# Kernel optimization log

Hardware: AMD Instinct MI355X
Metric: run time of the kernel (lower is better)

The kernel has to match this reference:

```python
import jax, jax.numpy as jnp
import numpy as np

TOKENS_PER_LAYER = 16  # v in rearrange 'b l (a v) -> b l a v'


def setup_inputs() -> dict:
    key = jax.random.key(0)
    k1, k2 = jax.random.split(key)
    vocab, embed_dim = 1024, 256
    x = jax.random.normal(k1, (64, 32, embed_dim * TOKENS_PER_LAYER), dtype=jnp.float32)
    # nn.Embedding init: uniform(-1/vocab, 1/vocab)
    emb_weight = jax.random.uniform(k2, (vocab, embed_dim), dtype=jnp.float32,
                                    minval=-1.0 / vocab, maxval=1.0 / vocab)
    return {"x": x, "emb_weight": emb_weight}


def reference(x, emb_weight):
    v = TOKENS_PER_LAYER
    b, l, av = x.shape
    a = av // v  # embed_dim
    # rearrange 'b l (a v) -> b l a v'
    z = x.reshape(b, l, a, v)
    # rearrange 'b l a v -> (b l v) a'
    z_flat = z.transpose(0, 1, 3, 2).reshape(b * l * v, a)
    # pairwise squared L2 distance via sum-of-squares + GEMM: [N, vocab]
    dist = (jnp.sum(z_flat * z_flat, axis=1, keepdims=True)
            + jnp.sum(emb_weight * emb_weight, axis=1)
            - 2.0 * (z_flat @ emb_weight.T))
    tokens = jnp.argmin(dist, axis=-1)  # [N] int
    # embedding gather, then rearrange '(b l v) e -> b l e v'
    z_q = emb_weight[tokens].reshape(b, l, v, a).transpose(0, 1, 3, 2)
    # straight-through decoder input: z + sg(z_q - z)
    decoder_input = z + jax.lax.stop_gradient(z_q - z)
    tokens = tokens.reshape(b, l, v)
    return z_q, decoder_input, tokens
```

## Files before the change

### kernel.cpp

```cpp
#include <hip/hip_runtime.h>


#define A_DIM 256
#define VOCAB 1024
#define NROWS 32768
#define ZQ_ELEMS ((size_t)8388608)
#define TAU_C 3.0e-4f
#define TAU_F 2.0e-4f

typedef _Float16 f16x8 __attribute__((ext_vector_type(8)));
typedef _Float16 f16x4 __attribute__((ext_vector_type(4)));
typedef float f32x4 __attribute__((ext_vector_type(4)));

#define WS_EHT   ((size_t)0)
#define WS_ZH    ((size_t)524288)
#define WS_ESQ   ((size_t)17301504)
#define WS_ZSQ   ((size_t)17305600)
#define WS_RINFO ((size_t)17436672)
#define WS_NEED  ((size_t)17960960)


__global__ __launch_bounds__(256) void prep_fused(const float* __restrict__ x,
                                                  const float* __restrict__ emb,
                                                  _Float16* __restrict__ zh,
                                                  float* __restrict__ zsq,
                                                  float* __restrict__ esq,
                                                  _Float16* __restrict__ eht) {
    __shared__ float raw[A_DIM * 17];
    const int tid = threadIdx.x;
    if (blockIdx.x >= 2048) {
        const int blk = blockIdx.x - 2048;
        const int j = blk * 16 + (tid & 15);
        const int sub = tid >> 4;
        const float4* row = (const float4*)(emb + (size_t)j * A_DIM);
        #pragma unroll
        for (int t = 0; t < 2; ++t) {
            int kb = sub * 2 + t;
            float4 e0 = row[kb * 2], e1 = row[kb * 2 + 1];
            f16x8 hh;
            hh[0] = (_Float16)e0.x; hh[1] = (_Float16)e0.y; hh[2] = (_Float16)e0.z; hh[3] = (_Float16)e0.w;
            hh[4] = (_Float16)e1.x; hh[5] = (_Float16)e1.y; hh[6] = (_Float16)e1.z; hh[7] = (_Float16)e1.w;
            *(f16x8*)(eht + ((size_t)kb * 1024 + j) * 8) = hh;
        }
        if (sub == 0) {
            double s = 0.0;
            #pragma unroll 4
            for (int t = 0; t < A_DIM / 4; ++t) {
                float4 f = row[t];
                float sx = f.x * f.x, sy = f.y * f.y, sz = f.z * f.z, sw = f.w * f.w;
                s += (double)sx + (double)sy + (double)sz + (double)sw;
            }
            esq[j] = (float)s;
        }
        return;
    }
    const int bl = blockIdx.x;
    #pragma unroll
    for (int t = 0; t < 4; ++t) {
        int f4 = tid * 4 + t * 1024;
        float4 val = *(const float4*)(x + (size_t)bl * 4096 + f4);
        int a = f4 >> 4, v0 = f4 & 15;
        raw[a * 17 + v0 + 0] = val.x;
        raw[a * 17 + v0 + 1] = val.y;
        raw[a * 17 + v0 + 2] = val.z;
        raw[a * 17 + v0 + 3] = val.w;
    }
    __syncthreads();
    #pragma unroll
    for (int t = 0; t < 4; ++t) {
        int p = tid + t * 256;
        int v = p >> 6, a0 = (p & 63) * 4;
        f16x4 hq;
        hq[0] = (_Float16)raw[(a0 + 0) * 17 + v];
        hq[1] = (_Float16)raw[(a0 + 1) * 17 + v];
        hq[2] = (_Float16)raw[(a0 + 2) * 17 + v];
        hq[3] = (_Float16)raw[(a0 + 3) * 17 + v];
        *(f16x4*)(zh + ((size_t)bl * 16 + v) * 256 + a0) = hq;
    }
    if (tid < 16) {
        double s = 0.0;
        for (int a = 0; a < A_DIM; ++a) {
            float zf = raw[a * 17 + tid];
            float z2 = zf * zf;
            s += (double)z2;
        }
        zsq[bl * 16 + tid] = (float)s;
    }
}

__global__ __launch_bounds__(256) void mfma_kernel(const _Float16* __restrict__ zh,
                                                   const _Float16* __restrict__ eht,
                                                   const float* __restrict__ esq_g,
                                                   int4* __restrict__ rowinfo) {
    __shared__ float t3buf[2][32][6];
    const int tid = threadIdx.x;
    const int wq = tid >> 6;
    const int lane = tid & 63;
    const int q = lane >> 4;
    const int ln = lane & 15;
    const int g = wq & 1;
    const int h = wq >> 1;
    const int row0 = blockIdx.x * 32 + g * 16;
    const int cbase = h * 512;

    f16x8 afr[8];
    #pragma unroll
    for (int kt = 0; kt < 8; ++kt)
        afr[kt] = *(const f16x8*)(zh + (size_t)(row0 + ln) * 256 + kt * 32 + q * 8);

    const f16x8* ep[8];
    #pragma unroll
    for (int kt = 0; kt < 8; ++kt)
        ep[kt] = (const f16x8*)(eht + ((size_t)(kt * 4 + q) * 1024 + cbase + ln) * 8);

    float tv1[4], tv2[4], tv3[4];
    int   ti1[4], ti2[4], ti3[4];
    #pragma unroll
    for (int s = 0; s < 4; ++s) {
        tv1[s] = 3.0e38f; tv2[s] = 3.0e38f; tv3[s] = 3.0e38f;
        ti1[s] = 0; ti2[s] = 0; ti3[s] = 0;
    }

    for (int ch = 0; ch < 32; ++ch) {
        f16x8 bfr[8];
        #pragma unroll
        for (int kt = 0; kt < 8; ++kt)
            bfr[kt] = ep[kt][(size_t)ch * 16];
        f32x4 a0 = (f32x4){0.f, 0.f, 0.f, 0.f};
        f32x4 a1 = (f32x4){0.f, 0.f, 0.f, 0.f};
        #pragma unroll
        for (int kt = 0; kt < 4; ++kt)
            a0 = __builtin_amdgcn_mfma_f32_16x16x32_f16(afr[kt], bfr[kt], a0, 0, 0, 0);
        #pragma unroll
        for (int kt = 4; kt < 8; ++kt)
            a1 = __builtin_amdgcn_mfma_f32_16x16x32_f16(afr[kt], bfr[kt], a1, 0, 0, 0);
        const int cand = cbase + ch * 16 + ln;
        float es = esq_g[cand];
        #pragma unroll
        for (int reg = 0; reg < 4; ++reg) {
            float s = fmaf(-2.0f, a0[reg] + a1[reg], es);
            if (s < tv3[reg]) {
                if (s < tv2[reg]) {
                    tv3[reg] = tv2[reg]; ti3[reg] = ti2[reg];
                    if (s < tv1[reg]) {
                        tv2[reg] = tv1[reg]; ti2[reg] = ti1[reg];
                        tv1[reg] = s; ti1[reg] = cand;
                    } else { tv2[reg] = s; ti2[reg] = cand; }
                } else { tv3[reg] = s; ti3[reg] = cand; }
            }
        }
    }

    #pragma unroll
    for (int slot = 0; slot < 4; ++slot) {
        float v1 = tv1[slot], v2 = tv2[slot], v3 = tv3[slot];
        int i1 = ti1[slot], i2 = ti2[slot], i3 = ti3[slot];
        #pragma unroll
        for (int m = 1; m <= 8; m <<= 1) {
            float ov1 = __shfl_xor(v1, m); int oi1 = __shfl_xor(i1, m);
            float ov2 = __shfl_xor(v2, m); int oi2 = __shfl_xor(i2, m);
            float ov3 = __shfl_xor(v3, m); int oi3 = __shfl_xor(i3, m);
            #define INS3(ov, oi)                                                         \
                if (ov < v3 || (ov == v3 && oi < i3)) {                                  \
                    if (ov < v2 || (ov == v2 && oi < i2)) {                              \
                        v3 = v2; i3 = i2;                                                \
                        if (ov < v1 || (ov == v1 && oi < i1)) {                          \
                            v2 = v1; i2 = i1; v1 = ov; i1 = oi;                          \
                        } else { v2 = ov; i2 = oi; }                                     \
                    } else { v3 = ov; i3 = oi; }                                         \
                }
            INS3(ov1, oi1)
            INS3(ov2, oi2)
            INS3(ov3, oi3)
            #undef INS3
        }
        if (ln == 0) {
            int rl = g * 16 + q * 4 + slot;
            float* hp = &t3buf[h][rl][0];
            hp[0] = v1; hp[1] = __int_as_float(i1);
            hp[2] = v2; hp[3] = __int_as_float(i2);
            hp[4] = v3; hp[5] = __int_as_float(i3);
        }
    }
    __syncthreads();

    if (tid < 32) {
        const float* h0 = &t3buf[0][tid][0];
        const float* h1 = &t3buf[1][tid][0];
        float v1 = h0[0]; int i1 = __float_as_int(h0[1]);
        float v2 = h0[2]; int i2 = __float_as_int(h0[3]);
        float v3 = h0[4]; int i3 = __float_as_int(h0[5]);
        #pragma unroll
        for (int e = 0; e < 3; ++e) {
            float ov = h1[2 * e]; int oi = __float_as_int(h1[2 * e + 1]);
            if (ov < v3 || (ov == v3 && oi < i3)) {
                if (ov < v2 || (ov == v2 && oi < i2)) {
                    v3 = v2; i3 = i2;
                    if (ov < v1 || (ov == v1 && oi < i1)) {
                        v2 = v1; i2 = i1; v1 = ov; i1 = oi;
                    } else { v2 = ov; i2 = oi; }
                } else { v3 = ov; i3 = oi; }
            }
        }
        int cls = 0;
        if (v2 - v1 <= TAU_C) cls = (v3 - v1 > TAU_C) ? 1 : 2;
        rowinfo[blockIdx.x * 32 + tid] = make_int4(i1, i2, cls, 0);
    }
}

__global__ __launch_bounds__(256) void finish_kernel(const float* __restrict__ x,
                                                     const float* __restrict__ emb,
                                                     const float* __restrict__ esq,
                                                     const float* __restrict__ zsq,
                                                     const int4* __restrict__ rowinfo,
                                                     float* __restrict__ out) {
    __shared__ int4 ri[16];
    __shared__ int ftok[16];
    __shared__ float zrow[A_DIM];
    __shared__ float wv[4];
    __shared__ int   wi[4];
    const int tid = threadIdx.x;
    const int wq = tid >> 6, lane = tid & 63;
    const int bl = blockIdx.x;

    if (tid < 16) {
        int4 e = rowinfo[bl * 16 + tid];
        ri[tid] = e;
        ftok[tid] = e.x;
    }
    __syncthreads();

    for (int j = 0; j < 16; ++j) {
        if (ri[j].z != 2) continue;
        const int r = bl * 16 + j;
        __syncthreads();
        zrow[tid] = x[(size_t)bl * 4096 + (size_t)tid * 16 + j];
        __syncthreads();
        const float4* e0 = (const float4*)(emb + (size_t)tid * 4 * A_DIM);
        double d0 = 0.0, d1 = 0.0, d2 = 0.0, d3 = 0.0;
        #pragma unroll 8
        for (int k4 = 0; k4 < A_DIM / 4; ++k4) {
            float4 zf = *(const float4*)&zrow[k4 * 4];
            double z0 = (double)zf.x, z1 = (double)zf.y;
            double z2 = (double)zf.z, z3 = (double)zf.w;
            float4 f0 = e0[k4];
            float4 f1 = e0[64 + k4];
            float4 f2 = e0[128 + k4];
            float4 f3 = e0[192 + k4];
            d0 = fma((double)f0.x, z0, d0); d0 = fma((double)f0.y, z1, d0);
            d0 = fma((double)f0.z, z2, d0); d0 = fma((double)f0.w, z3, d0);
            d1 = fma((double)f1.x, z0, d1); d1 = fma((double)f1.y, z1, d1);
            d1 = fma((double)f1.z, z2, d1); d1 = fma((double)f1.w, z3, d1);
            d2 = fma((double)f2.x, z0, d2); d2 = fma((double)f2.y, z1, d2);
            d2 = fma((double)f2.z, z2, d2); d2 = fma((double)f2.w, z3, d2);
            d3 = fma((double)f3.x, z0, d3); d3 = fma((double)f3.y, z1, d3);
            d3 = fma((double)f3.z, z2, d3); d3 = fma((double)f3.w, z3, d3);
        }
        const float zq = zsq[r];
        float bv = 3.0e38f; int bi = 0;
        double dd[4] = {d0, d1, d2, d3};
        #pragma unroll
        for (int cc = 0; cc < 4; ++cc) {
            int c = tid * 4 + cc;
            float A = zq + esq[c];
            float D = (float)(2.0 * dd[cc]);
            float s = A - D;
            if (s < bv) { bv = s; bi = c; }
        }
        #pragma unroll
        for (int m = 1; m < 64; m <<= 1) {
            float ov = __shfl_xor(bv, m); int oi = __shfl_xor(bi, m);
            if (ov < bv || (ov == bv && oi < bi)) { bv = ov; bi = oi; }
        }
        if (lane == 0) { wv[wq] = bv; wi[wq] = bi; }
        __syncthreads();
        if (tid == 0) {
            float BV = wv[0]; int BI = wi[0];
            #pragma unroll
            for (int t = 1; t < 4; ++t)
                if (wv[t] < BV || (wv[t] == BV && wi[t] < BI)) { BV = wv[t]; BI = wi[t]; }
            ftok[j] = BI;
        }
    }

    for (int j = wq; j < 16; j += 4) {
        if (ri[j].z != 1) continue;
        const int r = bl * 16 + j;
        const int c1 = ri[j].x, c2 = ri[j].y;
        const float* xr = x + (size_t)bl * 4096 + j;
        const float* e1 = emb + (size_t)c1 * A_DIM;
        const float* e2 = emb + (size_t)c2 * A_DIM;
        double d1 = 0.0, d2 = 0.0;
        #pragma unroll
        for (int k = 0; k < 4; ++k) {
            int a = lane + k * 64;
            double zv = (double)xr[a * 16];
            d1 = fma(zv, (double)e1[a], d1);
            d2 = fma(zv, (double)e2[a], d2);
        }
        #pragma unroll
        for (int m = 1; m < 64; m <<= 1) {
            d1 += __shfl_xor(d1, m);
            d2 += __shfl_xor(d2, m);
        }
        if (lane == 0) {
            float zq = zsq[r];
            float A1 = zq + esq[c1];
            float D1 = (float)(2.0 * d1);
            float s1 = A1 - D1;
            float A2 = zq + esq[c2];
            float D2 = (float)(2.0 * d2);
            float s2 = A2 - D2;
            int bi = (s2 < s1 || (s2 == s1 && c2 < c1)) ? c2 : c1;
            ftok[j] = bi;
        }
    }
    __syncthreads();

    if (tid < 16)
        out[2 * ZQ_ELEMS + (size_t)(bl * 16 + tid)] = (float)ftok[tid];
    float4* oz = (float4*)(out + (size_t)bl * 4096);
    float4* od = (float4*)(out + ZQ_ELEMS + (size_t)bl * 4096);
    #pragma unroll
    for (int t = 0; t < 4; ++t) {
        int p = tid + t * 256;
        int a = p >> 2, v0 = (p & 3) * 4;
        float4 val;
        val.x = emb[(size_t)ftok[v0 + 0] * A_DIM + a];
        val.y = emb[(size_t)ftok[v0 + 1] * A_DIM + a];
        val.z = emb[(size_t)ftok[v0 + 2] * A_DIM + a];
        val.w = emb[(size_t)ftok[v0 + 3] * A_DIM + a];
        oz[p] = val;
        od[p] = val;
    }
}


__global__ __launch_bounds__(256) void prep_f(const float* __restrict__ emb,
                                              float* __restrict__ e_sq32) {
    int j = blockIdx.x * 256 + threadIdx.x;
    if (j < VOCAB) {
        const float4* row = (const float4*)(emb + (size_t)j * A_DIM);
        double s = 0.0;
        #pragma unroll 4
        for (int t = 0; t < A_DIM / 4; ++t) {
            float4 f = row[t];
            float sx = f.x * f.x, sy = f.y * f.y, sz = f.z * f.z, sw = f.w * f.w;
            s += (double)sx + (double)sy + (double)sz + (double)sw;
        }
        e_sq32[j] = (float)s;
    }
}

#define FBM 64
#define FBN 256
#define FBK 32
struct SmemF {
    union {
        struct { float zs[FBK][FBM]; float es[FBK][FBN]; };
        float4 mbuf[FBM][32];
        struct { double zrow[A_DIM]; float rbest[256]; int ridx[256]; };
    };
    double zsqp_s[4][FBM];
    float  zsq[FBM];
    int    tok[FBM];
    int    flagrows[FBM];
    int    nflag;
};

__global__ __launch_bounds__(256, 2) void main_f(const float* __restrict__ x,
                                                 const float* __restrict__ emb,
                                                 const float* __restrict__ e_sq32,
                                                 float* __restrict__ out) {
    __shared__ SmemF sm;
    const int tid = threadIdx.x;
    const int tx = tid & 31;
    const int ty = tid >> 5;
    const int blk = blockIdx.x;
    const int row0 = blk * FBM;
    const int bl0 = row0 >> 4;
    const int zrow_id = tid & 63;
    const int zq4     = tid >> 6;

    if (tid == 0) sm.nflag = 0;
    float v1[8], v2[8];
    int   i1[8], i2[8];
    #pragma unroll
    for (int r = 0; r < 8; ++r) { v1[r] = 3.0e38f; v2[r] = 3.0e38f; i1[r] = 0; i2[r] = 0; }
    double zsqp = 0.0;
    float4 zpf[2];
    float4 epf[8];
    for (int ct = 0; ct < VOCAB / FBN; ++ct) {
        float acc[8][8];
        #pragma unroll
        for (int rr = 0; rr < 8; ++rr)
            #pragma unroll
            for (int cc = 0; cc < 8; ++cc) acc[rr][cc] = 0.0f;
        for (int kt = 0; kt < A_DIM / FBK; ++kt) {
            if (kt == 0) {
                #pragma unroll
                for (int t = 0; t < 2; ++t) {
                    int f = tid + t * 256;
                    int v4 = f & 3, g = (f >> 2) & 3, kk = f >> 4;
                    zpf[t] = *(const float4*)(x + (size_t)(bl0 + g) * 4096 + (kt * FBK + kk) * 16 + v4 * 4);
                }
                #pragma unroll
                for (int t = 0; t < 8; ++t) {
                    int f = tid + t * 256;
                    int c = f & 255, k4 = f >> 8;
                    epf[t] = *(const float4*)(emb + (size_t)(ct * FBN + c) * A_DIM + kt * FBK + k4 * 4);
                }
            }
            __syncthreads();
            #pragma unroll
            for (int t = 0; t < 2; ++t) {
                int f = tid + t * 256;
                int v4 = f & 3, g = (f >> 2) & 3, kk = f >> 4;
                *(float4*)&sm.zs[kk][g * 16 + v4 * 4] = zpf[t];
            }
            #pragma unroll
            for (int t = 0; t < 8; ++t) {
                int f = tid + t * 256;
                int c = f & 255, k4 = f >> 8;
                sm.es[k4 * 4 + 0][c] = epf[t].x;
                sm.es[k4 * 4 + 1][c] = epf[t].y;
                sm.es[k4 * 4 + 2][c] = epf[t].z;
                sm.es[k4 * 4 + 3][c] = epf[t].w;
            }
            __syncthreads();
            if (kt + 1 < A_DIM / FBK) {
                #pragma unroll
                for (int t = 0; t < 2; ++t) {
                    int f = tid + t * 256;
                    int v4 = f & 3, g = (f >> 2) & 3, kk = f >> 4;
                    zpf[t] = *(const float4*)(x + (size_t)(bl0 + g) * 4096 + ((kt + 1) * FBK + kk) * 16 + v4 * 4);
                }
                #pragma unroll
                for (int t = 0; t < 8; ++t) {
                    int f = tid + t * 256;
                    int c = f & 255, k4 = f >> 8;
                    epf[t] = *(const float4*)(emb + (size_t)(ct * FBN + c) * A_DIM + (kt + 1) * FBK + k4 * 4);
                }
            }
            if (ct == 0 && (kt >> 1) == zq4) {
                #pragma unroll
                for (int kk = 0; kk < FBK; ++kk) {
                    float zf = sm.zs[kk][zrow_id];
                    float zf2 = zf * zf;
                    zsqp += (double)zf2;
                }
            }
            #pragma unroll 2
            for (int kk = 0; kk < FBK; ++kk) {
                float4 za = *(float4*)&sm.zs[kk][ty * 4];
                float4 zb = *(float4*)&sm.zs[kk][32 + ty * 4];
                float4 ea = *(float4*)&sm.es[kk][tx * 4];
                float4 eb = *(float4*)&sm.es[kk][128 + tx * 4];
                float zv[8] = {za.x, za.y, za.z, za.w, zb.x, zb.y, zb.z, zb.w};
                float ev[8] = {ea.x, ea.y, ea.z, ea.w, eb.x, eb.y, eb.z, eb.w};
                #pragma unroll
                for (int rr = 0; rr < 8; ++rr)
                    #pragma unroll
                    for (int cc = 0; cc < 8; ++cc)
                        acc[rr][cc] = fmaf(zv[rr], ev[cc], acc[rr][cc]);
            }
        }
        if (ct == 0) {
            sm.zsqp_s[zq4][zrow_id] = zsqp;
            __syncthreads();
            if (tid < FBM)
                sm.zsq[tid] = (float)(sm.zsqp_s[0][tid] + sm.zsqp_s[1][tid]
                                    + sm.zsqp_s[2][tid] + sm.zsqp_s[3][tid]);
            __syncthreads();
        }
        float esqv[8];
        #pragma unroll
        for (int cc = 0; cc < 8; ++cc) {
            int c = ct * FBN + (cc >> 2) * 128 + tx * 4 + (cc & 3);
            esqv[cc] = e_sq32[c];
        }
        #pragma unroll
        for (int rr = 0; rr < 8; ++rr) {
            int R = (rr >> 2) * 32 + ty * 4 + (rr & 3);
            float zq = sm.zsq[R];
            #pragma unroll
            for (int cc = 0; cc < 8; ++cc) {
                int c = ct * FBN + (cc >> 2) * 128 + tx * 4 + (cc & 3);
                float A = zq + esqv[cc];
                float s = fmaf(-2.0f, acc[rr][cc], A);
                if (s < v1[rr]) { v2[rr] = v1[rr]; i2[rr] = i1[rr]; v1[rr] = s; i1[rr] = c; }
                else if (s < v2[rr]) { v2[rr] = s; i2[rr] = c; }
            }
        }
    }
    __syncthreads();
    #pragma unroll
    for (int rr = 0; rr < 8; ++rr) {
        int r = (rr >> 2) * 32 + ty * 4 + (rr & 3);
        float4 m;
        m.x = v1[rr]; m.y = __int_as_float(i1[rr]);
        m.z = v2[rr]; m.w = __int_as_float(i2[rr]);
        sm.mbuf[r][tx] = m;
    }
    __syncthreads();
    if (tid < FBM) {
        int r = tid;
        float V1 = 3.0e38f, V2 = 3.0e38f;
        int I1 = 0, I2 = 0;
        for (int t = 0; t < 32; ++t) {
            float4 m = sm.mbuf[r][t];
            float a1 = m.x; int a1i = __float_as_int(m.y);
            float a2 = m.z; int a2i = __float_as_int(m.w);
            if (a1 < V1 || (a1 == V1 && a1i < I1)) { V2 = V1; I2 = I1; V1 = a1; I1 = a1i; }
            else if (a1 < V2 || (a1 == V2 && a1i < I2)) { V2 = a1; I2 = a1i; }
            if (a2 < V1 || (a2 == V1 && a2i < I1)) { V2 = V1; I2 = I1; V1 = a2; I1 = a2i; }
            else if (a2 < V2 || (a2 == V2 && a2i < I2)) { V2 = a2; I2 = a2i; }
        }
        sm.tok[r] = I1;
        if (V2 - V1 <= TAU_F) {
            int pos = atomicAdd(&sm.nflag, 1);
            sm.flagrows[pos] = r;
        }
    }
    __syncthreads();
    const int nf = sm.nflag;
    for (int i = 0; i < nf; ++i) {
        const int rl = sm.flagrows[i];
        const int bl = bl0 + (rl >> 4);
        const int v  = rl & 15;
        const float zqrow = sm.zsq[rl];
        sm.zrow[tid] = (double)x[(size_t)bl * 4096 + (size_t)tid * 16 + v];
        __syncthreads();
        float bv = 3.0e38f; int bi = 0;
        #pragma unroll
        for (int cc = 0; cc < 4; ++cc) {
            int c = tid * 4 + cc;
            const float4* er = (const float4*)(emb + (size_t)c * A_DIM);
            double dot = 0.0;
            #pragma unroll 8
            for (int k4 = 0; k4 < A_DIM / 4; ++k4) {
                float4 f = er[k4];
                dot = fma((double)f.x, sm.zrow[k4 * 4 + 0], dot);
                dot = fma((double)f.y, sm.zrow[k4 * 4 + 1], dot);
                dot = fma((double)f.z, sm.zrow[k4 * 4 + 2], dot);
                dot = fma((double)f.w, sm.zrow[k4 * 4 + 3], dot);
            }
            float A = zqrow + e_sq32[c];
            float D = (float)(2.0 * dot);
            float s = A - D;
            if (s < bv) { bv = s; bi = c; }
        }
        sm.rbest[tid] = bv; sm.ridx[tid] = bi;
        __syncthreads();
        if (tid == 0) {
            float BV = sm.rbest[0]; int BI = sm.ridx[0];
            for (int t = 1; t < 256; ++t) {
                float vv = sm.rbest[t];
                if (vv < BV) { BV = vv; BI = sm.ridx[t]; }
            }
            sm.tok[rl] = BI;
        }
        __syncthreads();
    }
    if (tid < FBM) {
        out[2 * ZQ_ELEMS + (size_t)(row0 + tid)] = (float)sm.tok[tid];
    }
    __syncthreads();
    const int a = tid;
    for (int g = 0; g < 4; ++g) {
        __align__(16) float h[16];
        #pragma unroll
        for (int v = 0; v < 16; ++v) {
            h[v] = emb[(size_t)sm.tok[g * 16 + v] * A_DIM + a];
        }
        size_t base = ((size_t)(bl0 + g) * A_DIM + a) * 16;
        float4* p0 = (float4*)(out + base);
        float4* p1 = (float4*)(out + ZQ_ELEMS + base);
        #pragma unroll
        for (int qq = 0; qq < 4; ++qq) {
            float4 val = *(float4*)&h[qq * 4];
            p0[qq] = val;
            p1[qq] = val;
        }
    }
}

extern "C" void kernel_launch(void* const* d_in, const int* in_sizes, int n_in,
                              void* d_out, int out_size, void* d_ws, size_t ws_size,
                              hipStream_t stream) {
    (void)in_sizes; (void)n_in; (void)out_size;
    const float* x   = (const float*)d_in[0];
    const float* emb = (const float*)d_in[1];
    float* out = (float*)d_out;
    char* ws = (char*)d_ws;

    if (ws_size >= WS_NEED) {
        _Float16* eht = (_Float16*)(ws + WS_EHT);
        _Float16* zh  = (_Float16*)(ws + WS_ZH);
        float* esq    = (float*)(ws + WS_ESQ);
        float* zsq    = (float*)(ws + WS_ZSQ);
        int4* rinfo   = (int4*)(ws + WS_RINFO);

        prep_fused<<<2112, 256, 0, stream>>>(x, emb, zh, zsq, esq, eht);
        mfma_kernel<<<1024, 256, 0, stream>>>(zh, eht, esq, rinfo);
        finish_kernel<<<2048, 256, 0, stream>>>(x, emb, esq, zsq, rinfo, out);
    } else {
        float* e_sq32 = (float*)ws;
        prep_f<<<4, 256, 0, stream>>>(emb, e_sq32);
        main_f<<<512, 256, 0, stream>>>(x, emb, e_sq32, out);
    }
}
```

Measured before the change: 245.9 us.

## Split finish kernel into rescan over 64-row blocks and separate gather kernel

Splits the finish stage into two kernels. The first is a rescan kernel that handles ambiguous rows with 64 rows per block over 512 blocks and writes the final tokens to workspace. The second is a gather kernel over 2048 blocks that writes z_q and the decoder input from those tokens. This decouples the unevenly distributed exact rescans from the bandwidth-bound gather, so slow rescans no longer stall gather blocks. The cost is an extra launch, a small token buffer round trip, and fewer blocks for the rescan work, which may serialize more full-vocab rescans per block.

```diff
diff --git a/kernel.cpp b/kernel.cpp
--- a/kernel.cpp
+++ b/kernel.cpp
@@ -17,7 +17,8 @@
 #define WS_ESQ   ((size_t)17301504)
 #define WS_ZSQ   ((size_t)17305600)
 #define WS_RINFO ((size_t)17436672)
-#define WS_NEED  ((size_t)17960960)
+#define WS_TOK   ((size_t)17960960)
+#define WS_NEED  ((size_t)18092032)
 
 
 __global__ __launch_bounds__(256) void prep_fused(const float* __restrict__ x,
@@ -208,33 +209,34 @@
     }
 }
 
-__global__ __launch_bounds__(256) void finish_kernel(const float* __restrict__ x,
+__global__ __launch_bounds__(256) void rescan_kernel(const float* __restrict__ x,
                                                      const float* __restrict__ emb,
                                                      const float* __restrict__ esq,
                                                      const float* __restrict__ zsq,
                                                      const int4* __restrict__ rowinfo,
+                                                     int* __restrict__ tok,
                                                      float* __restrict__ out) {
-    __shared__ int4 ri[16];
-    __shared__ int ftok[16];
+    __shared__ int4 ri[64];
+    __shared__ int ftok[64];
     __shared__ float zrow[A_DIM];
     __shared__ float wv[4];
     __shared__ int   wi[4];
     const int tid = threadIdx.x;
     const int wq = tid >> 6, lane = tid & 63;
-    const int bl = blockIdx.x;
-
-    if (tid < 16) {
-        int4 e = rowinfo[bl * 16 + tid];
+    const int row0 = blockIdx.x * 64;
+
+    if (tid < 64) {
+        int4 e = rowinfo[row0 + tid];
         ri[tid] = e;
         ftok[tid] = e.x;
     }
     __syncthreads();
 
-    for (int j = 0; j < 16; ++j) {
+    for (int j = 0; j < 64; ++j) {
         if (ri[j].z != 2) continue;
-        const int r = bl * 16 + j;
+        const int r = row0 + j;
         __syncthreads();
-        zrow[tid] = x[(size_t)bl * 4096 + (size_t)tid * 16 + j];
+        zrow[tid] = x[(size_t)(r >> 4) * 4096 + (size_t)tid * 16 + (r & 15)];
         __syncthreads();
         const float4* e0 = (const float4*)(emb + (size_t)tid * 4 * A_DIM);
         double d0 = 0.0, d1 = 0.0, d2 = 0.0, d3 = 0.0;
@@ -283,11 +285,11 @@
         }
     }
 
-    for (int j = wq; j < 16; j += 4) {
+    for (int j = wq; j < 64; j += 4) {
         if (ri[j].z != 1) continue;
-        const int r = bl * 16 + j;
+        const int r = row0 + j;
         const int c1 = ri[j].x, c2 = ri[j].y;
-        const float* xr = x + (size_t)bl * 4096 + j;
+        const float* xr = x + (size_t)(r >> 4) * 4096 + (r & 15);
         const float* e1 = emb + (size_t)c1 * A_DIM;
         const float* e2 = emb + (size_t)c2 * A_DIM;
         double d1 = 0.0, d2 = 0.0;
@@ -317,8 +319,20 @@
     }
     __syncthreads();
 
-    if (tid < 16)
-        out[2 * ZQ_ELEMS + (size_t)(bl * 16 + tid)] = (float)ftok[tid];
+    if (tid < 64) {
+        tok[row0 + tid] = ftok[tid];
+        out[2 * ZQ_ELEMS + (size_t)(row0 + tid)] = (float)ftok[tid];
+    }
+}
+
+__global__ __launch_bounds__(256) void gather_kernel(const float* __restrict__ emb,
+                                                     const int* __restrict__ tok,
+                                                     float* __restrict__ out) {
+    __shared__ int t16[16];
+    const int tid = threadIdx.x;
+    const int bl = blockIdx.x;
+    if (tid < 16) t16[tid] = tok[bl * 16 + tid];
+    __syncthreads();
     float4* oz = (float4*)(out + (size_t)bl * 4096);
     float4* od = (float4*)(out + ZQ_ELEMS + (size_t)bl * 4096);
     #pragma unroll
@@ -326,10 +340,10 @@
         int p = tid + t * 256;
         int a = p >> 2, v0 = (p & 3) * 4;
         float4 val;
-        val.x = emb[(size_t)ftok[v0 + 0] * A_DIM + a];
-        val.y = emb[(size_t)ftok[v0 + 1] * A_DIM + a];
-        val.z = emb[(size_t)ftok[v0 + 2] * A_DIM + a];
-        val.w = emb[(size_t)ftok[v0 + 3] * A_DIM + a];
+        val.x = emb[(size_t)t16[v0 + 0] * A_DIM + a];
+        val.y = emb[(size_t)t16[v0 + 1] * A_DIM + a];
+        val.z = emb[(size_t)t16[v0 + 2] * A_DIM + a];
+        val.w = emb[(size_t)t16[v0 + 3] * A_DIM + a];
         oz[p] = val;
         od[p] = val;
     }
@@ -600,10 +614,12 @@
         float* esq    = (float*)(ws + WS_ESQ);
         float* zsq    = (float*)(ws + WS_ZSQ);
         int4* rinfo   = (int4*)(ws + WS_RINFO);
+        int* tok      = (int*)(ws + WS_TOK);
 
         prep_fused<<<2112, 256, 0, stream>>>(x, emb, zh, zsq, esq, eht);
         mfma_kernel<<<1024, 256, 0, stream>>>(zh, eht, esq, rinfo);
-        finish_kernel<<<2048, 256, 0, stream>>>(x, emb, esq, zsq, rinfo, out);
+        rescan_kernel<<<512, 256, 0, stream>>>(x, emb, esq, zsq, rinfo, tok, out);
+        gather_kernel<<<2048, 256, 0, stream>>>(emb, tok, out);
     } else {
         float* e_sq32 = (float*)ws;
         prep_f<<<4, 256, 0, stream>>>(emb, e_sq32);
```

Result: slower. 275.5 us (+12.0%).
